# Kernel tuning notes

Measured on AMD Instinct MI355X. Metric: run time of the kernel, lower is better.

Reference implementation:

```python
import jax, jax.numpy as jnp
import numpy as np

B, T, D, U = 64, 2048, 512, 512

def setup_inputs() -> dict:
    key = jax.random.key(0)
    ks = jax.random.split(key, 5)
    scale = 1.0 / np.sqrt(D)
    return {
        "features": jax.random.normal(ks[0], (B, T, D), dtype=jnp.float32),
        "hidden": jax.random.normal(ks[1], (B, D), dtype=jnp.float32),
        "W1": jax.random.normal(ks[2], (D, U), dtype=jnp.float32) * scale,
        "b1": jnp.zeros((U,), dtype=jnp.float32),
        "W2": jax.random.normal(ks[3], (D, U), dtype=jnp.float32) * scale,
        "b2": jnp.zeros((U,), dtype=jnp.float32),
        "V": jax.random.normal(ks[4], (U, 1), dtype=jnp.float32) * (1.0 / np.sqrt(U)),
        "bV": jnp.zeros((1,), dtype=jnp.float32),
    }

def reference(features, hidden, W1, b1, W2, b2, V, bV):
    # features: [B, T, D]; hidden: [B, D]
    proj_f = jnp.einsum('btd,du->btu', features, W1) + b1          # [B, T, U]
    proj_h = (hidden @ W2 + b2)[:, None, :]                        # [B, 1, U]
    score = jnp.tanh(proj_f + proj_h) @ V + bV                     # [B, T, 1]
    attention_weights = jax.nn.softmax(score, axis=1)              # [B, T, 1]
    context_vector = jnp.sum(attention_weights * features, axis=1) # [B, D]
    return (context_vector, attention_weights)
```

## Files before the change

kernel.cpp:

```cpp
#include <hip/hip_runtime.h>
#include <hip/hip_bf16.h>

#define BB 64
#define TT 2048
#define DD 512
#define UU 512
#define MM (BB * TT)
#define CTX_ELEMS (BB * DD)
#define ATTN_OFF  CTX_ELEMS

typedef __bf16 bf16x8 __attribute__((ext_vector_type(8)));
typedef float  f32x4  __attribute__((ext_vector_type(4)));
typedef unsigned short u16x8 __attribute__((ext_vector_type(8)));
typedef unsigned int u32;

#define GLOBAL_AS __attribute__((address_space(1)))
#define LDS_AS    __attribute__((address_space(3)))

__device__ __forceinline__ unsigned short f2bf(float f) {
    union { float f; unsigned u; } x; x.f = f;
    unsigned r = x.u + 0x7fffu + ((x.u >> 16) & 1u);
    return (unsigned short)(r >> 16);
}

__device__ __forceinline__ float tanh_fast(float x) {
    x = fminf(fmaxf(x, -10.f), 10.f);
    float e = __builtin_amdgcn_exp2f(x * 2.885390082f);
    return (e - 1.0f) * __builtin_amdgcn_rcpf(e + 1.0f);
}

__global__ void k_w1t(const float* __restrict__ W1, unsigned short* __restrict__ W1T) {
    int gid = blockIdx.x * 256 + threadIdx.x;
    int u  = gid & 511;
    int dc = gid >> 9;
    int d0 = dc * 8;
    u16x8 pk;
    #pragma unroll
    for (int e = 0; e < 8; ++e)
        pk[e] = f2bf(W1[(size_t)(d0 + e) * UU + u]);
    int nt = u >> 7, n = u & 127;
    int kt = dc >> 2, kc = dc & 3;
    size_t off = ((size_t)(nt * 16 + kt) * 8192 + kc * 2048 + n * 16) / 2;
    *(u16x8*)(W1T + off) = pk;
}

__global__ void k_phc(const float* __restrict__ hidden, const float* __restrict__ W2,
                      const float* __restrict__ b1, const float* __restrict__ b2,
                      float* __restrict__ phc) {
    const int b = blockIdx.x;
    const int u = threadIdx.x;
    const float* h = hidden + (size_t)b * DD;
    float acc = b1[u] + b2[u];
    #pragma unroll 8
    for (int d = 0; d < DD; ++d)
        acc += h[d] * W2[(size_t)d * UU + u];
    phc[(size_t)b * UU + u] = acc;
}

__launch_bounds__(256, 3)
__global__ void k_score(const float* __restrict__ feat,
                        const unsigned short* __restrict__ W1T,
                        const float* __restrict__ phc,
                        const float* __restrict__ V,
                        float* __restrict__ part) {
    __shared__ float sA[128 * 32];
    __shared__ unsigned short sB[4096];
    __shared__ float sRed[4][64];

    const int tid  = threadIdx.x;
    const int lane = tid & 63;
    const int w    = tid >> 6;
    const int wr   = w >> 1, wc = w & 1;

    const int rb  = blockIdx.x;
    const int xcd = rb & 7;
    const int uu  = rb >> 3;
    const int gy  = uu & 3;
    const int gx  = xcd * 128 + (uu >> 2);
    const int m0  = gx * 128;
    const int b   = m0 >> 11;

    f32x4 acc[4][4];
    #pragma unroll
    for (int i = 0; i < 4; ++i)
        #pragma unroll
        for (int j = 0; j < 4; ++j)
            acc[i][j] = (f32x4){0.f, 0.f, 0.f, 0.f};

    const char* fbase0 = (const char*)feat + (size_t)m0 * 2048;
    const char* bslab0 = (const char*)W1T + (size_t)gy * 16 * 8192;

    for (int kt = 0; kt < 16; ++kt) {
        const char* bslab = bslab0 + kt * 8192;
        #pragma unroll
        for (int p = 0; p < 2; ++p) {
            int s = p * 256 + tid;
            const char* src = bslab + s * 16;
            char* dst = (char*)sB + (size_t)(p * 256 + (tid & ~63)) * 16;
            __builtin_amdgcn_global_load_lds((const GLOBAL_AS u32*)src, (LDS_AS u32*)dst, 16, 0, 0);
        }
        const char* fbase = fbase0 + kt * 128;
        #pragma unroll
        for (int j = 0; j < 4; ++j) {
            int s = j * 256 + tid;
            int row = s >> 3;
            int cpos = s & 7;
            int c = cpos ^ (row & 7);
            const char* src = fbase + (size_t)row * 2048 + c * 16;
            char* dst = (char*)sA + (size_t)(j * 256 + (tid & ~63)) * 16;
            __builtin_amdgcn_global_load_lds((const GLOBAL_AS u32*)src, (LDS_AS u32*)dst, 16, 0, 0);
        }
        __syncthreads();

        const int kc = lane >> 4;
        bf16x8 bfr[4];
        #pragma unroll
        for (int ns = 0; ns < 4; ++ns) {
            int n = wc * 64 + ns * 16 + (lane & 15);
            bfr[ns] = *(const bf16x8*)((const char*)sB + kc * 2048 + n * 16);
        }
        #pragma unroll
        for (int ms = 0; ms < 4; ++ms) {
            int m = wr * 64 + ms * 16 + (lane & 15);
            int c0 = (2 * kc) ^ (m & 7);
            int c1 = (2 * kc + 1) ^ (m & 7);
            f32x4 a0 = *(const f32x4*)((const char*)sA + m * 128 + c0 * 16);
            f32x4 a1 = *(const f32x4*)((const char*)sA + m * 128 + c1 * 16);
            bf16x8 af;
            #pragma unroll
            for (int j = 0; j < 4; ++j) { af[j] = (__bf16)a0[j]; af[4 + j] = (__bf16)a1[j]; }
            #pragma unroll
            for (int ns = 0; ns < 4; ++ns)
                acc[ms][ns] = __builtin_amdgcn_mfma_f32_16x16x32_bf16(af, bfr[ns], acc[ms][ns], 0, 0, 0);
        }
        __syncthreads();
    }

    float pc[4], vv[4];
    #pragma unroll
    for (int ns = 0; ns < 4; ++ns) {
        int ug = gy * 128 + wc * 64 + ns * 16 + (lane & 15);
        pc[ns] = phc[(size_t)b * UU + ug];
        vv[ns] = V[ug];
    }
    float pr[4][4];
    #pragma unroll
    for (int ms = 0; ms < 4; ++ms)
        #pragma unroll
        for (int rg = 0; rg < 4; ++rg) {
            float s = 0.f;
            #pragma unroll
            for (int ns = 0; ns < 4; ++ns)
                s += tanh_fast(acc[ms][ns][rg] + pc[ns]) * vv[ns];
            pr[ms][rg] = s;
        }
    #pragma unroll
    for (int off = 1; off < 16; off <<= 1)
        #pragma unroll
        for (int ms = 0; ms < 4; ++ms)
            #pragma unroll
            for (int rg = 0; rg < 4; ++rg)
                pr[ms][rg] += __shfl_xor(pr[ms][rg], off, 64);
    if ((lane & 15) == 0) {
        int rowg = lane >> 4;
        #pragma unroll
        for (int ms = 0; ms < 4; ++ms)
            #pragma unroll
            for (int rg = 0; rg < 4; ++rg)
                sRed[w][ms * 16 + rowg * 4 + rg] = pr[ms][rg];
    }
    __syncthreads();
    if (tid < 128) {
        int wrx = tid >> 6, ml = tid & 63;
        float v = sRed[2 * wrx][ml] + sRed[2 * wrx + 1][ml];
        part[(size_t)gy * MM + m0 + tid] = v;
    }
}

__global__ void k_softmax(const float* __restrict__ part, float* __restrict__ dout) {
    const int b = blockIdx.x, tid = threadIdx.x;
    float* sc = dout + ATTN_OFF + (size_t)b * TT;
    float v[8];
    float mx = -3.4e38f;
    #pragma unroll
    for (int i = 0; i < 8; ++i) {
        int t = tid + 256 * i;
        size_t idx = (size_t)b * TT + t;
        v[i] = part[idx] + part[MM + idx] + part[2 * MM + idx] + part[3 * MM + idx];
        mx = fmaxf(mx, v[i]);
    }
    __shared__ float red[256];
    red[tid] = mx; __syncthreads();
    for (int s = 128; s >= 1; s >>= 1) {
        if (tid < s) red[tid] = fmaxf(red[tid], red[tid + s]);
        __syncthreads();
    }
    mx = red[0]; __syncthreads();
    float sum = 0.f;
    #pragma unroll
    for (int i = 0; i < 8; ++i) { v[i] = __expf(v[i] - mx); sum += v[i]; }
    red[tid] = sum; __syncthreads();
    for (int s = 128; s >= 1; s >>= 1) {
        if (tid < s) red[tid] += red[tid + s];
        __syncthreads();
    }
    float inv = 1.0f / red[0];
    #pragma unroll
    for (int i = 0; i < 8; ++i) sc[tid + 256 * i] = v[i] * inv;
}

__global__ void k_context(const float* __restrict__ feat, float* __restrict__ dout) {
    const int b = blockIdx.x, dc = blockIdx.y;
    const int dq = threadIdx.x & 15;
    const int ty = threadIdx.x >> 4;
    const int d = dc * 64 + dq * 4;
    const float* wgt = dout + ATTN_OFF + (size_t)b * TT;
    const float* f = feat + (size_t)b * TT * DD + d;
    float4 acc = {0.f, 0.f, 0.f, 0.f};
    #pragma unroll 4
    for (int i = 0; i < TT / 16; ++i) {
        int t = i * 16 + ty;
        float wv = wgt[t];
        float4 fv = *(const float4*)(f + (size_t)t * DD);
        acc.x += wv * fv.x; acc.y += wv * fv.y;
        acc.z += wv * fv.z; acc.w += wv * fv.w;
    }
    __shared__ float4 red[16][16];
    red[ty][dq] = acc; __syncthreads();
    if (ty == 0) {
        float4 s = red[0][dq];
        #pragma unroll
        for (int k = 1; k < 16; ++k) {
            float4 r = red[k][dq];
            s.x += r.x; s.y += r.y; s.z += r.z; s.w += r.w;
        }
        *(float4*)(dout + (size_t)b * DD + d) = s;
    }
}

extern "C" void kernel_launch(void* const* d_in, const int* in_sizes, int n_in,
                              void* d_out, int out_size, void* d_ws, size_t ws_size,
                              hipStream_t stream) {
    (void)in_sizes; (void)n_in; (void)out_size; (void)ws_size;
    const float* feat   = (const float*)d_in[0];
    const float* hidden = (const float*)d_in[1];
    const float* W1     = (const float*)d_in[2];
    const float* b1     = (const float*)d_in[3];
    const float* W2     = (const float*)d_in[4];
    const float* b2     = (const float*)d_in[5];
    const float* V      = (const float*)d_in[6];

    unsigned short* W1T = (unsigned short*)d_ws;
    float* phc  = (float*)((char*)d_ws + 512 * 1024);
    float* part = (float*)((char*)d_ws + 640 * 1024);
    float* out  = (float*)d_out;

    hipLaunchKernelGGL(k_w1t,     dim3(128),    dim3(256), 0, stream, W1, W1T);
    hipLaunchKernelGGL(k_phc,     dim3(64),     dim3(512), 0, stream, hidden, W2, b1, b2, phc);
    hipLaunchKernelGGL(k_score,   dim3(4096),   dim3(256), 0, stream, feat, W1T, phc, V, part);
    hipLaunchKernelGGL(k_softmax, dim3(64),     dim3(256), 0, stream, part, out);
    hipLaunchKernelGGL(k_context, dim3(64, 8),  dim3(256), 0, stream, feat, out);
}
```

Measured before the change: 196.0 us.

## Double-buffer score GEMM with register-staged bf16 A tile and prefetch

The score kernel gets double-buffered LDS tiles. The next B slab is loaded asynchronously and the next fp32 feature chunk is fetched into registers while the current tile's MFMAs run. The A tile is now converted to bf16 once per thread when written to LDS, instead of every wave reading fp32 from LDS and converting per fragment. This halves A's LDS footprint and removes one barrier per iteration. Occupancy is raised to 4 blocks per CU and MFMA issue priority is raised. The extra register staging may raise register pressure under the tighter launch bound.

Result: no change. 195.0 us (-0.5%).

```diff
diff --git a/kernel.cpp b/kernel.cpp
--- a/kernel.cpp
+++ b/kernel.cpp
@@ -57,14 +57,14 @@
     phc[(size_t)b * UU + u] = acc;
 }
 
-__launch_bounds__(256, 3)
+__launch_bounds__(256, 4)
 __global__ void k_score(const float* __restrict__ feat,
                         const unsigned short* __restrict__ W1T,
                         const float* __restrict__ phc,
                         const float* __restrict__ V,
                         float* __restrict__ part) {
-    __shared__ float sA[128 * 32];
-    __shared__ unsigned short sB[4096];
+    __shared__ __align__(16) unsigned short sA[2][4096];
+    __shared__ __align__(16) unsigned short sB[2][4096];
     __shared__ float sRed[4][64];
 
     const int tid  = threadIdx.x;
@@ -80,6 +80,43 @@
     const int m0  = gx * 128;
     const int b   = m0 >> 11;
 
+    const char* bslab0 = (const char*)W1T + (size_t)gy * 16 * 8192;
+    const char* fbase0 = (const char*)feat + (size_t)m0 * 2048;
+
+    const int r = tid >> 1;
+    const int h = tid & 1;
+    const char* fA = fbase0 + (size_t)r * 2048 + h * 64;
+
+    f32x4 areg0, areg1, areg2, areg3;
+
+    #define STAGE_B(buf, kt_) {                                                   \
+        const char* bs = bslab0 + (kt_) * 8192;                                   \
+        _Pragma("unroll")                                                         \
+        for (int p = 0; p < 2; ++p) {                                             \
+            const char* src = bs + (size_t)(p * 256 + tid) * 16;                  \
+            char* dst = (char*)&sB[buf][0] + (size_t)(p * 256 + (tid & ~63)) * 16;\
+            __builtin_amdgcn_global_load_lds((const GLOBAL_AS u32*)src,           \
+                                             (LDS_AS u32*)dst, 16, 0, 0);         \
+        }                                                                         \
+    }
+    #define LOAD_A(kt_) {                                                         \
+        const char* s_ = fA + (kt_) * 128;                                        \
+        areg0 = *(const f32x4*)(s_);                                              \
+        areg1 = *(const f32x4*)(s_ + 16);                                         \
+        areg2 = *(const f32x4*)(s_ + 32);                                         \
+        areg3 = *(const f32x4*)(s_ + 48);                                         \
+    }
+    #define WRITE_A(buf) {                                                        \
+        bf16x8 p0, p1;                                                            \
+        _Pragma("unroll")                                                         \
+        for (int j = 0; j < 4; ++j) {                                             \
+            p0[j] = (__bf16)areg0[j]; p0[4 + j] = (__bf16)areg1[j];               \
+            p1[j] = (__bf16)areg2[j]; p1[4 + j] = (__bf16)areg3[j];               \
+        }                                                                         \
+        *(bf16x8*)((char*)&sA[buf][0] + (2 * h) * 2048 + r * 16) = p0;            \
+        *(bf16x8*)((char*)&sA[buf][0] + (2 * h + 1) * 2048 + r * 16) = p1;        \
+    }
+
     f32x4 acc[4][4];
     #pragma unroll
     for (int i = 0; i < 4; ++i)
@@ -87,54 +124,40 @@
         for (int j = 0; j < 4; ++j)
             acc[i][j] = (f32x4){0.f, 0.f, 0.f, 0.f};
 
-    const char* fbase0 = (const char*)feat + (size_t)m0 * 2048;
-    const char* bslab0 = (const char*)W1T + (size_t)gy * 16 * 8192;
+    STAGE_B(0, 0);
+    LOAD_A(0);
+    WRITE_A(0);
+    __syncthreads();
 
     for (int kt = 0; kt < 16; ++kt) {
-        const char* bslab = bslab0 + kt * 8192;
-        #pragma unroll
-        for (int p = 0; p < 2; ++p) {
-            int s = p * 256 + tid;
-            const char* src = bslab + s * 16;
-            char* dst = (char*)sB + (size_t)(p * 256 + (tid & ~63)) * 16;
-            __builtin_amdgcn_global_load_lds((const GLOBAL_AS u32*)src, (LDS_AS u32*)dst, 16, 0, 0);
+        const int cur = kt & 1;
+        if (kt < 15) {
+            STAGE_B(cur ^ 1, kt + 1);
+            LOAD_A(kt + 1);
         }
-        const char* fbase = fbase0 + kt * 128;
-        #pragma unroll
-        for (int j = 0; j < 4; ++j) {
-            int s = j * 256 + tid;
-            int row = s >> 3;
-            int cpos = s & 7;
-            int c = cpos ^ (row & 7);
-            const char* src = fbase + (size_t)row * 2048 + c * 16;
-            char* dst = (char*)sA + (size_t)(j * 256 + (tid & ~63)) * 16;
-            __builtin_amdgcn_global_load_lds((const GLOBAL_AS u32*)src, (LDS_AS u32*)dst, 16, 0, 0);
-        }
+        const int kc = lane >> 4;
+        bf16x8 bfr[4], af[4];
+        #pragma unroll
+        for (int ns = 0; ns < 4; ++ns)
+            bfr[ns] = *(const bf16x8*)((const char*)&sB[cur][0] + kc * 2048 +
+                                       (wc * 64 + ns * 16 + (lane & 15)) * 16);
+        #pragma unroll
+        for (int ms = 0; ms < 4; ++ms)
+            af[ms] = *(const bf16x8*)((const char*)&sA[cur][0] + kc * 2048 +
+                                      (wr * 64 + ms * 16 + (lane & 15)) * 16);
+        __builtin_amdgcn_s_setprio(1);
+        #pragma unroll
+        for (int ms = 0; ms < 4; ++ms)
+            #pragma unroll
+            for (int ns = 0; ns < 4; ++ns)
+                acc[ms][ns] = __builtin_amdgcn_mfma_f32_16x16x32_bf16(af[ms], bfr[ns], acc[ms][ns], 0, 0, 0);
+        __builtin_amdgcn_s_setprio(0);
+        if (kt < 15) WRITE_A(cur ^ 1);
         __syncthreads();
-
-        const int kc = lane >> 4;
-        bf16x8 bfr[4];
-        #pragma unroll
-        for (int ns = 0; ns < 4; ++ns) {
-            int n = wc * 64 + ns * 16 + (lane & 15);
-            bfr[ns] = *(const bf16x8*)((const char*)sB + kc * 2048 + n * 16);
-        }
-        #pragma unroll
-        for (int ms = 0; ms < 4; ++ms) {
-            int m = wr * 64 + ms * 16 + (lane & 15);
-            int c0 = (2 * kc) ^ (m & 7);
-            int c1 = (2 * kc + 1) ^ (m & 7);
-            f32x4 a0 = *(const f32x4*)((const char*)sA + m * 128 + c0 * 16);
-            f32x4 a1 = *(const f32x4*)((const char*)sA + m * 128 + c1 * 16);
-            bf16x8 af;
-            #pragma unroll
-            for (int j = 0; j < 4; ++j) { af[j] = (__bf16)a0[j]; af[4 + j] = (__bf16)a1[j]; }
-            #pragma unroll
-            for (int ns = 0; ns < 4; ++ns)
-                acc[ms][ns] = __builtin_amdgcn_mfma_f32_16x16x32_bf16(af, bfr[ns], acc[ms][ns], 0, 0, 0);
-        }
-        __syncthreads();
-    }
+    }
+    #undef STAGE_B
+    #undef LOAD_A
+    #undef WRITE_A
 
     float pc[4], vv[4];
     #pragma unroll
```

## Triple-buffer GEMM mainloop with register-staged bf16 A tiles and one barrier per step

Applied to the files above, without the earlier changes.

Rewrites the k_score mainloop as a fully unrolled three-stage software pipeline. B tiles go asynchronously into a triple-buffered LDS, while A (fp32 features) is loaded into registers two steps ahead, converted to bf16 once and written to LDS in a k-major layout. Fragment reads become single bf16x8 loads, and the loop uses one barrier per step with manual waitcnt and setprio around the MFMAs. It should hide global latency and remove the per-fragment fp32-to-bf16 conversion from the LDS path, at the cost of more LDS (about 48KB), more registers and fragile hand-placed waitcnts that may cut occupancy below the 3 blocks per SM requested by launch bounds.

Result: no change. 195.5 us (-0.2%).

```diff
diff --git a/kernel.cpp b/kernel.cpp
--- a/kernel.cpp
+++ b/kernel.cpp
@@ -63,8 +63,8 @@
                         const float* __restrict__ phc,
                         const float* __restrict__ V,
                         float* __restrict__ part) {
-    __shared__ float sA[128 * 32];
-    __shared__ unsigned short sB[4096];
+    __shared__ __align__(16) unsigned short sA[3 * 4096];
+    __shared__ __align__(16) unsigned short sB[3 * 4096];
     __shared__ float sRed[4][64];
 
     const int tid  = threadIdx.x;
@@ -80,6 +80,15 @@
     const int m0  = gx * 128;
     const int b   = m0 >> 11;
 
+    const char* bslab0 = (const char*)W1T + (size_t)gy * 16 * 8192;
+    const char* fbase0 = (const char*)feat + (size_t)m0 * 2048;
+
+    const int r = tid >> 1;
+    const int h = tid & 1;
+    const char* fA = fbase0 + (size_t)r * 2048 + h * 64;
+
+    f32x4 pA0, pA1, pA2, pA3, pB0, pB1, pB2, pB3;
+
     f32x4 acc[4][4];
     #pragma unroll
     for (int i = 0; i < 4; ++i)
@@ -87,54 +96,101 @@
         for (int j = 0; j < 4; ++j)
             acc[i][j] = (f32x4){0.f, 0.f, 0.f, 0.f};
 
-    const char* fbase0 = (const char*)feat + (size_t)m0 * 2048;
-    const char* bslab0 = (const char*)W1T + (size_t)gy * 16 * 8192;
-
-    for (int kt = 0; kt < 16; ++kt) {
-        const char* bslab = bslab0 + kt * 8192;
-        #pragma unroll
-        for (int p = 0; p < 2; ++p) {
-            int s = p * 256 + tid;
-            const char* src = bslab + s * 16;
-            char* dst = (char*)sB + (size_t)(p * 256 + (tid & ~63)) * 16;
-            __builtin_amdgcn_global_load_lds((const GLOBAL_AS u32*)src, (LDS_AS u32*)dst, 16, 0, 0);
-        }
-        const char* fbase = fbase0 + kt * 128;
-        #pragma unroll
-        for (int j = 0; j < 4; ++j) {
-            int s = j * 256 + tid;
-            int row = s >> 3;
-            int cpos = s & 7;
-            int c = cpos ^ (row & 7);
-            const char* src = fbase + (size_t)row * 2048 + c * 16;
-            char* dst = (char*)sA + (size_t)(j * 256 + (tid & ~63)) * 16;
-            __builtin_amdgcn_global_load_lds((const GLOBAL_AS u32*)src, (LDS_AS u32*)dst, 16, 0, 0);
-        }
-        __syncthreads();
-
-        const int kc = lane >> 4;
-        bf16x8 bfr[4];
-        #pragma unroll
-        for (int ns = 0; ns < 4; ++ns) {
-            int n = wc * 64 + ns * 16 + (lane & 15);
-            bfr[ns] = *(const bf16x8*)((const char*)sB + kc * 2048 + n * 16);
-        }
-        #pragma unroll
-        for (int ms = 0; ms < 4; ++ms) {
-            int m = wr * 64 + ms * 16 + (lane & 15);
-            int c0 = (2 * kc) ^ (m & 7);
-            int c1 = (2 * kc + 1) ^ (m & 7);
-            f32x4 a0 = *(const f32x4*)((const char*)sA + m * 128 + c0 * 16);
-            f32x4 a1 = *(const f32x4*)((const char*)sA + m * 128 + c1 * 16);
-            bf16x8 af;
-            #pragma unroll
-            for (int j = 0; j < 4; ++j) { af[j] = (__bf16)a0[j]; af[4 + j] = (__bf16)a1[j]; }
-            #pragma unroll
-            for (int ns = 0; ns < 4; ++ns)
-                acc[ms][ns] = __builtin_amdgcn_mfma_f32_16x16x32_bf16(af, bfr[ns], acc[ms][ns], 0, 0, 0);
-        }
-        __syncthreads();
-    }
+#define VM6()   asm volatile("s_waitcnt vmcnt(6)" ::: "memory")
+#define VM0()   asm volatile("s_waitcnt vmcnt(0)" ::: "memory")
+#define LGKM0() asm volatile("s_waitcnt lgkmcnt(0)" ::: "memory")
+#define BAR()   __builtin_amdgcn_s_barrier()
+
+#define STAGE_B(bufi_, kt_) do {                                                   \
+    const char* bs_ = bslab0 + (kt_) * 8192;                                       \
+    _Pragma("unroll")                                                              \
+    for (int p_ = 0; p_ < 2; ++p_) {                                               \
+        const char* src_ = bs_ + (size_t)(p_ * 256 + tid) * 16;                    \
+        char* dst_ = (char*)sB + (bufi_) * 8192 + (size_t)(p_ * 256 + (tid & ~63)) * 16; \
+        __builtin_amdgcn_global_load_lds((const GLOBAL_AS u32*)src_,               \
+                                         (LDS_AS u32*)dst_, 16, 0, 0);             \
+    } } while (0)
+
+#define LOAD_A(P, kt_) do {                                                        \
+    const char* s_ = fA + (kt_) * 128;                                             \
+    P##0 = *(const f32x4*)(s_);                                                    \
+    P##1 = *(const f32x4*)(s_ + 16);                                               \
+    P##2 = *(const f32x4*)(s_ + 32);                                               \
+    P##3 = *(const f32x4*)(s_ + 48); } while (0)
+
+#define WRITE_A(bufi_, P) do {                                                     \
+    bf16x8 q0_, q1_;                                                               \
+    _Pragma("unroll")                                                              \
+    for (int j_ = 0; j_ < 4; ++j_) {                                               \
+        q0_[j_] = (__bf16)P##0[j_]; q0_[4 + j_] = (__bf16)P##1[j_];                \
+        q1_[j_] = (__bf16)P##2[j_]; q1_[4 + j_] = (__bf16)P##3[j_];                \
+    }                                                                              \
+    *(bf16x8*)((char*)sA + (bufi_) * 8192 + (2 * h) * 2048 + r * 16) = q0_;        \
+    *(bf16x8*)((char*)sA + (bufi_) * 8192 + (2 * h + 1) * 2048 + r * 16) = q1_; } while (0)
+
+#define FRAG_READ(c0_) do {                                                        \
+    const int kc_ = lane >> 4;                                                     \
+    _Pragma("unroll")                                                              \
+    for (int ns_ = 0; ns_ < 4; ++ns_)                                              \
+        bfr[ns_] = *(const bf16x8*)((const char*)sB + (c0_) * 8192 + kc_ * 2048 +  \
+                                    (wc * 64 + ns_ * 16 + (lane & 15)) * 16);      \
+    _Pragma("unroll")                                                              \
+    for (int ms_ = 0; ms_ < 4; ++ms_)                                              \
+        af[ms_] = *(const bf16x8*)((const char*)sA + (c0_) * 8192 + kc_ * 2048 +   \
+                                   (wr * 64 + ms_ * 16 + (lane & 15)) * 16); } while (0)
+
+#define MFMA_DO() do {                                                             \
+    __builtin_amdgcn_s_setprio(1);                                                 \
+    _Pragma("unroll")                                                              \
+    for (int ms_ = 0; ms_ < 4; ++ms_)                                              \
+        _Pragma("unroll")                                                          \
+        for (int ns_ = 0; ns_ < 4; ++ns_)                                          \
+            acc[ms_][ns_] = __builtin_amdgcn_mfma_f32_16x16x32_bf16(af[ms_], bfr[ns_], acc[ms_][ns_], 0, 0, 0); \
+    __builtin_amdgcn_s_setprio(0); } while (0)
+
+#define BODY(kt_, RA, RB, PRE, LAST)  do {                                         \
+    bf16x8 af[4], bfr[4];                                                          \
+    FRAG_READ((kt_) % 3);                                                          \
+    if (PRE) { STAGE_B(((kt_) + 2) % 3, (kt_) + 2); LOAD_A(RB, (kt_) + 2); }       \
+    MFMA_DO();                                                                     \
+    if (LAST) { VM0(); } else { VM6(); }                                           \
+    WRITE_A(((kt_) + 1) % 3, RA);                                                  \
+    LGKM0();                                                                       \
+    BAR(); } while (0)
+
+    STAGE_B(0, 0);
+    LOAD_A(pB, 0);
+    STAGE_B(1, 1);
+    LOAD_A(pA, 1);
+    VM6();
+    WRITE_A(0, pB);
+    LGKM0();
+    BAR();
+
+    BODY(0,  pA, pB, 1, 0);  BODY(1,  pB, pA, 1, 0);
+    BODY(2,  pA, pB, 1, 0);  BODY(3,  pB, pA, 1, 0);
+    BODY(4,  pA, pB, 1, 0);  BODY(5,  pB, pA, 1, 0);
+    BODY(6,  pA, pB, 1, 0);  BODY(7,  pB, pA, 1, 0);
+    BODY(8,  pA, pB, 1, 0);  BODY(9,  pB, pA, 1, 0);
+    BODY(10, pA, pB, 1, 0);  BODY(11, pB, pA, 1, 0);
+    BODY(12, pA, pB, 1, 0);  BODY(13, pB, pA, 1, 0);
+    BODY(14, pA, pB, 0, 1);
+    {
+        bf16x8 af[4], bfr[4];
+        FRAG_READ(0);
+        MFMA_DO();
+    }
+
+#undef BODY
+#undef MFMA_DO
+#undef FRAG_READ
+#undef WRITE_A
+#undef LOAD_A
+#undef STAGE_B
+#undef VM6
+#undef VM0
+#undef LGKM0
+#undef BAR
 
     float pc[4], vv[4];
     #pragma unroll
```

## Make score GEMM persistent with resident W1 slab and register-prefetched features

Applied to the files above, without the earlier changes.

The score kernel becomes persistent: 256 blocks of 512 threads each load their full 128-column bf16 W1 slab (128 KB) into LDS once. Each block then loops over 8 row tiles of one batch. Feature fragments are loaded straight from global memory into registers with a triple-buffered prefetch two k-steps ahead, replacing the per-k-step LDS staging and its two barriers. This aims to remove repeated W1 reloads and sync stalls, in exchange for one block per CU, a large LDS footprint, high register pressure, and uncoalesced 32-byte-per-lane global reads.

Result: slower. 440.3 us (+124.7%).

```diff
diff --git a/kernel.cpp b/kernel.cpp
--- a/kernel.cpp
+++ b/kernel.cpp
@@ -57,85 +57,31 @@
     phc[(size_t)b * UU + u] = acc;
 }
 
-__launch_bounds__(256, 3)
+__launch_bounds__(512, 1)
 __global__ void k_score(const float* __restrict__ feat,
                         const unsigned short* __restrict__ W1T,
                         const float* __restrict__ phc,
                         const float* __restrict__ V,
                         float* __restrict__ part) {
-    __shared__ float sA[128 * 32];
-    __shared__ unsigned short sB[4096];
-    __shared__ float sRed[4][64];
+    __shared__ __align__(16) unsigned short sB[16 * 4096];
+    __shared__ float sRed[8][64];
 
     const int tid  = threadIdx.x;
     const int lane = tid & 63;
     const int w    = tid >> 6;
-    const int wr   = w >> 1, wc = w & 1;
-
-    const int rb  = blockIdx.x;
-    const int xcd = rb & 7;
-    const int uu  = rb >> 3;
-    const int gy  = uu & 3;
-    const int gx  = xcd * 128 + (uu >> 2);
-    const int m0  = gx * 128;
-    const int b   = m0 >> 11;
-
-    f32x4 acc[4][4];
-    #pragma unroll
-    for (int i = 0; i < 4; ++i)
-        #pragma unroll
-        for (int j = 0; j < 4; ++j)
-            acc[i][j] = (f32x4){0.f, 0.f, 0.f, 0.f};
-
-    const char* fbase0 = (const char*)feat + (size_t)m0 * 2048;
-    const char* bslab0 = (const char*)W1T + (size_t)gy * 16 * 8192;
-
-    for (int kt = 0; kt < 16; ++kt) {
-        const char* bslab = bslab0 + kt * 8192;
-        #pragma unroll
-        for (int p = 0; p < 2; ++p) {
-            int s = p * 256 + tid;
-            const char* src = bslab + s * 16;
-            char* dst = (char*)sB + (size_t)(p * 256 + (tid & ~63)) * 16;
-            __builtin_amdgcn_global_load_lds((const GLOBAL_AS u32*)src, (LDS_AS u32*)dst, 16, 0, 0);
-        }
-        const char* fbase = fbase0 + kt * 128;
-        #pragma unroll
-        for (int j = 0; j < 4; ++j) {
-            int s = j * 256 + tid;
-            int row = s >> 3;
-            int cpos = s & 7;
-            int c = cpos ^ (row & 7);
-            const char* src = fbase + (size_t)row * 2048 + c * 16;
-            char* dst = (char*)sA + (size_t)(j * 256 + (tid & ~63)) * 16;
-            __builtin_amdgcn_global_load_lds((const GLOBAL_AS u32*)src, (LDS_AS u32*)dst, 16, 0, 0);
-        }
-        __syncthreads();
-
-        const int kc = lane >> 4;
-        bf16x8 bfr[4];
-        #pragma unroll
-        for (int ns = 0; ns < 4; ++ns) {
-            int n = wc * 64 + ns * 16 + (lane & 15);
-            bfr[ns] = *(const bf16x8*)((const char*)sB + kc * 2048 + n * 16);
-        }
-        #pragma unroll
-        for (int ms = 0; ms < 4; ++ms) {
-            int m = wr * 64 + ms * 16 + (lane & 15);
-            int c0 = (2 * kc) ^ (m & 7);
-            int c1 = (2 * kc + 1) ^ (m & 7);
-            f32x4 a0 = *(const f32x4*)((const char*)sA + m * 128 + c0 * 16);
-            f32x4 a1 = *(const f32x4*)((const char*)sA + m * 128 + c1 * 16);
-            bf16x8 af;
-            #pragma unroll
-            for (int j = 0; j < 4; ++j) { af[j] = (__bf16)a0[j]; af[4 + j] = (__bf16)a1[j]; }
-            #pragma unroll
-            for (int ns = 0; ns < 4; ++ns)
-                acc[ms][ns] = __builtin_amdgcn_mfma_f32_16x16x32_bf16(af, bfr[ns], acc[ms][ns], 0, 0, 0);
-        }
-        __syncthreads();
-    }
-
+    const int wm   = w >> 1, wc = w & 1;
+
+    const int bid = blockIdx.x;
+    const int b   = (bid & 7) + 8 * (bid >> 5);
+    const int gy  = (bid >> 3) & 3;
+
+    const char* bslab = (const char*)W1T + (size_t)gy * 131072;
+    #pragma unroll
+    for (int p = 0; p < 16; ++p) {
+        const char* src = bslab + (size_t)(p * 512 + tid) * 16;
+        char* dst = (char*)sB + (size_t)(p * 512 + (tid & ~63)) * 16;
+        __builtin_amdgcn_global_load_lds((const GLOBAL_AS u32*)src, (LDS_AS u32*)dst, 16, 0, 0);
+    }
     float pc[4], vv[4];
     #pragma unroll
     for (int ns = 0; ns < 4; ++ns) {
@@ -143,38 +89,132 @@
         pc[ns] = phc[(size_t)b * UU + ug];
         vv[ns] = V[ug];
     }
-    float pr[4][4];
-    #pragma unroll
-    for (int ms = 0; ms < 4; ++ms)
+    __syncthreads();
+
+    const int kcl   = lane >> 4;
+    const int rlane = lane & 15;
+    const char* fb0 = (const char*)feat +
+        ((size_t)(b * TT) + wm * 64 + rlane) * 2048 + kcl * 32;
+
+    f32x4 s0_[8], s1_[8], s2_[8];
+
+#define LOADA(S, ab0_, ab1_, ab2_, ab3_, kt_) do {                    \
+    S[0] = *(const f32x4*)((ab0_) + (kt_) * 128);                     \
+    S[1] = *(const f32x4*)((ab0_) + (kt_) * 128 + 16);                \
+    S[2] = *(const f32x4*)((ab1_) + (kt_) * 128);                     \
+    S[3] = *(const f32x4*)((ab1_) + (kt_) * 128 + 16);                \
+    S[4] = *(const f32x4*)((ab2_) + (kt_) * 128);                     \
+    S[5] = *(const f32x4*)((ab2_) + (kt_) * 128 + 16);                \
+    S[6] = *(const f32x4*)((ab3_) + (kt_) * 128);                     \
+    S[7] = *(const f32x4*)((ab3_) + (kt_) * 128 + 16); } while (0)
+
+#define KSTEP(kt_, CUR) do {                                          \
+    bf16x8 bfr[4];                                                    \
+    _Pragma("unroll")                                                 \
+    for (int ns_ = 0; ns_ < 4; ++ns_)                                 \
+        bfr[ns_] = *(const bf16x8*)((const char*)sB + (kt_) * 8192 +  \
+                    kcl * 2048 + (wc * 64 + ns_ * 16 + rlane) * 16);  \
+    _Pragma("unroll")                                                 \
+    for (int ms_ = 0; ms_ < 4; ++ms_) {                               \
+        bf16x8 af_;                                                   \
+        _Pragma("unroll")                                             \
+        for (int j_ = 0; j_ < 4; ++j_) {                              \
+            af_[j_]     = (__bf16)CUR[2 * ms_][j_];                   \
+            af_[4 + j_] = (__bf16)CUR[2 * ms_ + 1][j_];               \
+        }                                                             \
+        _Pragma("unroll")                                             \
+        for (int ns_ = 0; ns_ < 4; ++ns_)                             \
+            acc[ms_][ns_] = __builtin_amdgcn_mfma_f32_16x16x32_bf16(  \
+                af_, bfr[ns_], acc[ms_][ns_], 0, 0, 0);               \
+    } } while (0)
+
+    {
+        const char* a0 = fb0;
+        const char* a1 = fb0 + 16 * 2048;
+        const char* a2 = fb0 + 32 * 2048;
+        const char* a3 = fb0 + 48 * 2048;
+        LOADA(s0_, a0, a1, a2, a3, 0);
+        LOADA(s1_, a0, a1, a2, a3, 1);
+    }
+
+    for (int mt = 0; mt < 8; ++mt) {
+        const char* a0 = fb0 + (size_t)mt * 256 * 2048;
+        const char* a1 = a0 + 16 * 2048;
+        const char* a2 = a0 + 32 * 2048;
+        const char* a3 = a0 + 48 * 2048;
+
+        f32x4 acc[4][4];
         #pragma unroll
-        for (int rg = 0; rg < 4; ++rg) {
-            float s = 0.f;
-            #pragma unroll
-            for (int ns = 0; ns < 4; ++ns)
-                s += tanh_fast(acc[ms][ns][rg] + pc[ns]) * vv[ns];
-            pr[ms][rg] = s;
+        for (int i = 0; i < 4; ++i)
+            #pragma unroll
+            for (int j = 0; j < 4; ++j)
+                acc[i][j] = (f32x4){0.f, 0.f, 0.f, 0.f};
+
+        KSTEP(0,  s0_); LOADA(s2_, a0, a1, a2, a3, 2);
+        KSTEP(1,  s1_); LOADA(s0_, a0, a1, a2, a3, 3);
+        KSTEP(2,  s2_); LOADA(s1_, a0, a1, a2, a3, 4);
+        KSTEP(3,  s0_); LOADA(s2_, a0, a1, a2, a3, 5);
+        KSTEP(4,  s1_); LOADA(s0_, a0, a1, a2, a3, 6);
+        KSTEP(5,  s2_); LOADA(s1_, a0, a1, a2, a3, 7);
+        KSTEP(6,  s0_); LOADA(s2_, a0, a1, a2, a3, 8);
+        KSTEP(7,  s1_); LOADA(s0_, a0, a1, a2, a3, 9);
+        KSTEP(8,  s2_); LOADA(s1_, a0, a1, a2, a3, 10);
+        KSTEP(9,  s0_); LOADA(s2_, a0, a1, a2, a3, 11);
+        KSTEP(10, s1_); LOADA(s0_, a0, a1, a2, a3, 12);
+        KSTEP(11, s2_); LOADA(s1_, a0, a1, a2, a3, 13);
+        KSTEP(12, s0_); LOADA(s2_, a0, a1, a2, a3, 14);
+        KSTEP(13, s1_); LOADA(s0_, a0, a1, a2, a3, 15);
+        KSTEP(14, s2_);
+        if (mt < 7) {
+            const char* n0 = a0 + 256 * 2048;
+            const char* n1 = n0 + 16 * 2048;
+            const char* n2 = n0 + 32 * 2048;
+            const char* n3 = n0 + 48 * 2048;
+            KSTEP(15, s0_);
+            LOADA(s1_, n0, n1, n2, n3, 0);
+            LOADA(s2_, n0, n1, n2, n3, 1);
+            #pragma unroll
+            for (int q = 0; q < 8; ++q) { s0_[q] = s1_[q]; s1_[q] = s2_[q]; }
+        } else {
+            KSTEP(15, s0_);
         }
-    #pragma unroll
-    for (int off = 1; off < 16; off <<= 1)
+
+        float pr[4][4];
         #pragma unroll
         for (int ms = 0; ms < 4; ++ms)
             #pragma unroll
-            for (int rg = 0; rg < 4; ++rg)
-                pr[ms][rg] += __shfl_xor(pr[ms][rg], off, 64);
-    if ((lane & 15) == 0) {
-        int rowg = lane >> 4;
+            for (int rg = 0; rg < 4; ++rg) {
+                float s = 0.f;
+                #pragma unroll
+                for (int ns = 0; ns < 4; ++ns)
+                    s += tanh_fast(acc[ms][ns][rg] + pc[ns]) * vv[ns];
+                pr[ms][rg] = s;
+            }
         #pragma unroll
-        for (int ms = 0; ms < 4; ++ms)
-            #pragma unroll
-            for (int rg = 0; rg < 4; ++rg)
-                sRed[w][ms * 16 + rowg * 4 + rg] = pr[ms][rg];
-    }
-    __syncthreads();
-    if (tid < 128) {
-        int wrx = tid >> 6, ml = tid & 63;
-        float v = sRed[2 * wrx][ml] + sRed[2 * wrx + 1][ml];
-        part[(size_t)gy * MM + m0 + tid] = v;
-    }
+        for (int off = 1; off < 16; off <<= 1)
+            #pragma unroll
+            for (int ms = 0; ms < 4; ++ms)
+                #pragma unroll
+                for (int rg = 0; rg < 4; ++rg)
+                    pr[ms][rg] += __shfl_xor(pr[ms][rg], off, 64);
+        if ((lane & 15) == 0) {
+            int rowg = lane >> 4;
+            #pragma unroll
+            for (int ms = 0; ms < 4; ++ms)
+                #pragma unroll
+                for (int rg = 0; rg < 4; ++rg)
+                    sRed[w][ms * 16 + rowg * 4 + rg] = pr[ms][rg];
+        }
+        __syncthreads();
+        if (tid < 256) {
+            int wmx = tid >> 6, r = tid & 63;
+            float v = sRed[2 * wmx][r] + sRed[2 * wmx + 1][r];
+            part[(size_t)gy * MM + (size_t)b * TT + mt * 256 + tid] = v;
+        }
+        __syncthreads();
+    }
+#undef KSTEP
+#undef LOADA
 }
 
 __global__ void k_softmax(const float* __restrict__ part, float* __restrict__ dout) {
@@ -257,7 +297,7 @@
 
     hipLaunchKernelGGL(k_w1t,     dim3(128),    dim3(256), 0, stream, W1, W1T);
     hipLaunchKernelGGL(k_phc,     dim3(64),     dim3(512), 0, stream, hidden, W2, b1, b2, phc);
-    hipLaunchKernelGGL(k_score,   dim3(4096),   dim3(256), 0, stream, feat, W1T, phc, V, part);
+    hipLaunchKernelGGL(k_score,   dim3(256),    dim3(512), 0, stream, feat, W1T, phc, V, part);
     hipLaunchKernelGGL(k_softmax, dim3(64),     dim3(256), 0, stream, part, out);
     hipLaunchKernelGGL(k_context, dim3(64, 8),  dim3(256), 0, stream, feat, out);
 }
```
